# Kernel tuning notes

Hardware: AMD Instinct MI355X
Metric: run time of the kernel (lower is better)

Reference implementation:

```python
import jax, jax.numpy as jnp
import numpy as np

N_NODES = 50000
N_EDGES = 800000
DIM = 128
N_LAYERS = 4
EPS = 1e-5  # BatchNorm1d default eps


def setup_inputs() -> dict:
    key = jax.random.key(0)
    k_x, k_e, k_w = jax.random.split(key, 3)
    x = jax.random.normal(k_x, (N_NODES, DIM), dtype=jnp.float32)
    edge_index = jax.random.randint(k_e, (2, N_EDGES), 0, N_NODES, dtype=jnp.int32)
    # stacked per-layer params (input_dim == hidden_dim == DIM)
    Ws = jax.random.normal(k_w, (N_LAYERS, DIM, DIM), dtype=jnp.float32) * (1.0 / np.sqrt(DIM))
    bs = jnp.zeros((N_LAYERS, DIM), jnp.float32)
    gammas = jnp.ones((N_LAYERS, DIM), jnp.float32)
    betas = jnp.zeros((N_LAYERS, DIM), jnp.float32)
    return {"x": x, "edge_index": edge_index, "Ws": Ws, "bs": bs,
            "gammas": gammas, "betas": betas}


def gcn_conv(x, W, b, src, dst, n):
    # PyG GCNConv: h = X W; out = D^{-1/2}(A+I)D^{-1/2} h + b
    h = x @ W                                       # [N, D]
    deg = jnp.zeros((n,), h.dtype).at[dst].add(1.0) + 1.0  # +1 self-loop
    dis = jax.lax.rsqrt(deg)                        # deg > 0 due to self-loops
    msg = h[src] * (dis[src] * dis[dst])[:, None]   # [E, D] gather + scale
    out = jnp.zeros_like(h).at[dst].add(msg)        # scatter-add aggregate
    out = out + h * (dis * dis)[:, None]            # self-loop term, norm = 1/deg
    return out + b


def batchnorm(z, gamma, beta):
    # BatchNorm1d training-mode math: batch mean, biased variance
    mu = z.mean(axis=0)
    var = z.var(axis=0)
    return (z - mu) * jax.lax.rsqrt(var + EPS) * gamma + beta


def reference(x, edge_index, Ws, bs, gammas, betas):
    src, dst = edge_index[0], edge_index[1]
    z = x
    for i in range(N_LAYERS):
        z = gcn_conv(z, Ws[i], bs[i], src, dst, z.shape[0])
        z = jax.nn.relu(z)
        z = batchnorm(z, gammas[i], betas[i])
        # Dropout: identity (eval mode / deterministic reference)
    return z
```

## Files before the change

kernel.cpp:

```cpp
#include <hip/hip_runtime.h>

#define N_NODES 50000
#define N_EDGES 800000
#define DIM 128
#define NLAYERS 4
#define BN_EPS 1e-5f
#define SCAN_BLOCKS 196
#define WS2 72

typedef __attribute__((ext_vector_type(8))) short short8;
typedef __attribute__((ext_vector_type(4))) float f32x4;

__device__ __forceinline__ float bf2f(unsigned short u){
    union { unsigned int i; float f; } x; x.i = ((unsigned int)u) << 16; return x.f;
}
__device__ __forceinline__ unsigned short f2bf(float f){
    union { float f; unsigned int i; } x; x.f = f;
    unsigned int lsb = (x.i >> 16) & 1u;
    unsigned int r = x.i + 0x7fffu + lsb;
    return (unsigned short)(r >> 16);
}

struct P4 { int2 a, b, c, d; };

__device__ __forceinline__ P4 loadP_mask(const int2* __restrict__ ep, int base,
                                         int sub, int lim){
    P4 p;
    int i0 = base + sub, i1 = base + 4 + sub, i2 = base + 8 + sub, i3 = base + 12 + sub;
    p.a = (i0 < lim) ? ep[i0] : make_int2(0, 0);
    p.b = (i1 < lim) ? ep[i1] : make_int2(0, 0);
    p.c = (i2 < lim) ? ep[i2] : make_int2(0, 0);
    p.d = (i3 < lim) ? ep[i3] : make_int2(0, 0);
    return p;
}
__device__ __forceinline__ P4 loadP_full(const int2* __restrict__ ep, int base,
                                         int sub){
    P4 p;
    p.a = ep[base + sub];
    p.b = ep[base + 4 + sub];
    p.c = ep[base + 8 + sub];
    p.d = ep[base + 12 + sub];
    return p;
}
__device__ __forceinline__ P4 loadP(const int2* __restrict__ ep, int base,
                                    int sub, int lim){
    if (lim - base >= 16) return loadP_full(ep, base, sub);
    return loadP_mask(ep, base, sub, lim);
}


__global__ __launch_bounds__(256) void k_zero(int* __restrict__ p, int n){
    int i = blockIdx.x * 256 + threadIdx.x;
    if (i < n) p[i] = 0;
}

__global__ __launch_bounds__(256) void k_count(const int* __restrict__ dst,
                                               int* __restrict__ degcnt){
    int e = blockIdx.x * 256 + threadIdx.x;
    if (e < N_EDGES) atomicAdd(&degcnt[dst[e]], 1);
}

__global__ __launch_bounds__(256) void k_scan1(const int* __restrict__ degcnt,
                                               int* __restrict__ rowptr,
                                               int* __restrict__ bsum,
                                               float* __restrict__ dis){
    __shared__ int tmp[256];
    int t = threadIdx.x;
    int i = blockIdx.x * 256 + t;
    int v = (i < N_NODES) ? degcnt[i] : 0;
    if (i < N_NODES) dis[i] = rsqrtf((float)v + 1.0f);
    tmp[t] = v;
    __syncthreads();
    #pragma unroll
    for (int off = 1; off < 256; off <<= 1){
        int u = (t >= off) ? tmp[t - off] : 0;
        __syncthreads();
        tmp[t] += u;
        __syncthreads();
    }
    if (i < N_NODES) rowptr[i] = tmp[t] - v;
    if (t == 255) bsum[blockIdx.x] = tmp[255];
}

__global__ __launch_bounds__(256) void k_scan3(const int* __restrict__ bsum,
                                               int* __restrict__ rowptr,
                                               int* __restrict__ wptr){
    __shared__ int tmp[256];
    int t = threadIdx.x;
    int v = (t < SCAN_BLOCKS) ? bsum[t] : 0;
    tmp[t] = v;
    __syncthreads();
    #pragma unroll
    for (int off = 1; off < 256; off <<= 1){
        int u = (t >= off) ? tmp[t - off] : 0;
        __syncthreads();
        tmp[t] += u;
        __syncthreads();
    }
    int boff = (blockIdx.x == 0) ? 0 : tmp[blockIdx.x - 1];
    int i = blockIdx.x * 256 + t;
    if (i < N_NODES){
        int r = rowptr[i] + boff;
        rowptr[i] = r; wptr[i] = r;
    }
    if (i == 0) rowptr[N_NODES] = N_EDGES;
}

__global__ __launch_bounds__(256) void k_fill(const int* __restrict__ src,
                                              const int* __restrict__ dst,
                                              const float* __restrict__ dis,
                                              int* __restrict__ wptr,
                                              int2* __restrict__ epair){
    int e = blockIdx.x * 256 + threadIdx.x;
    if (e < N_EDGES){
        int s = src[e], d = dst[e];
        float w = dis[s] * dis[d];
        int p = atomicAdd(&wptr[d], 1);
        int2 pr; pr.x = s; pr.y = __float_as_int(w);
        epair[p] = pr;
    }
}


template<int MODE>
__global__ __launch_bounds__(256) void k_wprep(const float* __restrict__ W,
                                               const float* __restrict__ stats,
                                               const float* __restrict__ gamma,
                                               const float* __restrict__ beta,
                                               short* __restrict__ whip,
                                               short* __restrict__ wlop,
                                               float* __restrict__ b2g){
    __shared__ float scs[DIM], shs[DIM];
    __shared__ float part[256];
    int tid = threadIdx.x;
    if (MODE == 1){
        if (tid < DIM){
            float mu  = stats[tid] * (1.0f / N_NODES);
            float var = stats[DIM + tid] * (1.0f / N_NODES) - mu * mu;
            float sc  = rsqrtf(var + BN_EPS) * gamma[tid];
            scs[tid] = sc;
            shs[tid] = beta[tid] - mu * sc;
        }
        __syncthreads();
    }
    if (blockIdx.x < 16){
        int j = blockIdx.x * 1024 + tid * 4;
        int k = j >> 7;
        int c0 = j & 127;
        float4 wv = *(const float4*)(W + k*DIM + c0);
        float sc = (MODE == 1) ? scs[k] : 1.0f;
        float v[4] = {wv.x*sc, wv.y*sc, wv.z*sc, wv.w*sc};
        int h = k >> 6, kk = k & 63;
        #pragma unroll
        for (int i = 0; i < 4; i++){
            unsigned short hi = f2bf(v[i]);
            float lo = v[i] - bf2f(hi);
            int d = h*8192 + (c0 + i)*64 + kk;
            whip[d] = (short)hi;
            wlop[d] = (short)f2bf(lo);
        }
    } else {
        if (MODE == 0){
            if (tid < DIM) b2g[tid] = 0.f;
        } else {
            int c = tid >> 1, hf = tid & 1;
            float acc = 0.f;
            int k0 = hf * 64;
            #pragma unroll 4
            for (int k = k0; k < k0 + 64; k++)
                acc = fmaf(shs[k], W[k*DIM + c], acc);
            part[tid] = acc;
            __syncthreads();
            if (tid < DIM) b2g[tid] = part[2*tid] + part[2*tid + 1];
        }
    }
}

template<int MODE>
__global__ __launch_bounds__(256) void k_gemm(const void* __restrict__ zraw,
                                              const short* __restrict__ whip,
                                              const short* __restrict__ wlop,
                                              const float* __restrict__ b2g,
                                              unsigned short* __restrict__ hb){
    __shared__ short whi[DIM * WS2];
    __shared__ short wlo[DIM * WS2];
    __shared__ float b2s[DIM];
    int tid = threadIdx.x;

    int lane = tid & 63;
    int wv   = tid >> 6;
    int m = lane & 15;
    int q = lane >> 4;
    int row0 = blockIdx.x * 64 + wv * 16;
    int arow = row0 + m;
    bool avalid = arow < N_NODES;

    f32x4 acc[8];
    #pragma unroll
    for (int t = 0; t < 8; t++) acc[t] = (f32x4){0.f, 0.f, 0.f, 0.f};

    int cs = tid >> 1, pp = tid & 1;

    #pragma unroll
    for (int half = 0; half < 2; half++){
        {
            const short8* sh_ = (const short8*)(whip + half*8192 + cs*64 + pp*32);
            const short8* sl_ = (const short8*)(wlop + half*8192 + cs*64 + pp*32);
            short8* dh = (short8*)&whi[cs*WS2 + pp*32];
            short8* dl = (short8*)&wlo[cs*WS2 + pp*32];
            dh[0] = sh_[0]; dh[1] = sh_[1]; dh[2] = sh_[2]; dh[3] = sh_[3];
            dl[0] = sl_[0]; dl[1] = sl_[1]; dl[2] = sl_[2]; dl[3] = sl_[3];
            if (half == 0 && tid < DIM) b2s[tid] = b2g[tid];
        }
        __syncthreads();

        #pragma unroll
        for (int gl2 = 0; gl2 < 2; gl2++){
            int gg = half*2 + gl2;
            short8 a = {0,0,0,0,0,0,0,0};
            if (avalid){
                if (MODE == 0){
                    const float* xp = (const float*)zraw + (size_t)arow*DIM + gg*32 + q*8;
                    float4 v0 = *(const float4*)xp;
                    float4 v1 = *(const float4*)(xp + 4);
                    a[0] = (short)f2bf(v0.x); a[1] = (short)f2bf(v0.y);
                    a[2] = (short)f2bf(v0.z); a[3] = (short)f2bf(v0.w);
                    a[4] = (short)f2bf(v1.x); a[5] = (short)f2bf(v1.y);
                    a[6] = (short)f2bf(v1.z); a[7] = (short)f2bf(v1.w);
                } else {
                    a = *(const short8*)((const unsigned short*)zraw
                          + (size_t)gg*N_NODES*32 + (size_t)arow*32 + q*8);
                }
            }
            #pragma unroll
            for (int t = 0; t < 8; t++){
                int col = t*16 + m;
                int off = col*WS2 + gl2*32 + q*8;
                short8 bh = *(const short8*)&whi[off];
                short8 bl = *(const short8*)&wlo[off];
                acc[t] = __builtin_amdgcn_mfma_f32_16x16x32_bf16(a, bh, acc[t], 0, 0, 0);
                acc[t] = __builtin_amdgcn_mfma_f32_16x16x32_bf16(a, bl, acc[t], 0, 0, 0);
            }
        }
        if (half == 0) __syncthreads();
    }

    #pragma unroll
    for (int t = 0; t < 8; t++){
        int colg = t*16 + m;
        float bz = b2s[colg];
        size_t base = (size_t)(t >> 1)*N_NODES*32 + (t & 1)*16 + m;
        #pragma unroll
        for (int r = 0; r < 4; r++){
            int row = row0 + q*4 + r;
            if (row < N_NODES)
                hb[base + (size_t)row*32] = f2bf(acc[t][r] + bz);
        }
    }
}

__global__ __launch_bounds__(256) void k_agg(const unsigned short* __restrict__ h,
                                             const int* __restrict__ rowptr,
                                             const int2* __restrict__ epair,
                                             const float* __restrict__ dis,
                                             const float* __restrict__ bias,
                                             unsigned short* __restrict__ out,
                                             float* __restrict__ stats){
    int lane = threadIdx.x & 63;
    int w    = threadIdx.x >> 6;
    int g    = blockIdx.x & 3;
    int sub  = lane >> 4;
    int cp   = lane & 15;
    const ushort2* hg = (const ushort2*)(h + (size_t)g * N_NODES * 32);
    ushort2* og = (ushort2*)(out + (size_t)g * N_NODES * 32);
    float b0 = bias[g*32 + 2*cp], b1 = bias[g*32 + 2*cp + 1];
    float s0 = 0.f, s1 = 0.f, q0 = 0.f, q1 = 0.f;
    int bg = blockIdx.x >> 2;
    int nstride = (gridDim.x >> 2) * 4;

    int node = bg*4 + w;
    int ne0 = 0, ne1 = 0;
    ushort2 nhv; nhv.x = 0; nhv.y = 0;
    float ndi = 0.f;
    P4 nP = {{0,0},{0,0},{0,0},{0,0}};
    if (node < N_NODES){
        ne0 = rowptr[node];
        ne1 = rowptr[node + 1];
        nhv = hg[node*16 + cp];
        ndi = dis[node];
        nP  = loadP(epair, ne0, sub, ne1);
    }

    while (node < N_NODES){
        int e0 = ne0, e1 = ne1;
        ushort2 hv = nhv;
        float di = ndi;
        P4 P = nP;

        int nnext = node + nstride;
        if (nnext < N_NODES){
            ne0 = rowptr[nnext];
            ne1 = rowptr[nnext + 1];
            nhv = hg[nnext*16 + cp];
            ndi = dis[nnext];
        } else { ne0 = 0; ne1 = 0; }

        float pa0 = 0.f, pa1 = 0.f, pb0 = 0.f, pb1 = 0.f;
        float pc0 = 0.f, pc1 = 0.f, pd0 = 0.f, pd1 = 0.f;
        if (sub == 0){
            float dii = di * di;
            pa0 = bf2f(hv.x) * dii; pa1 = bf2f(hv.y) * dii;
        }

        int e = e0;
        while (e < e1){
            int en = e + 16;
            P4 Pn = {{0,0},{0,0},{0,0},{0,0}};
            if (en < e1) Pn = loadP(epair, en, sub, e1);
            ushort2 X0 = hg[P.a.x*16 + cp];
            ushort2 X1 = hg[P.b.x*16 + cp];
            ushort2 X2 = hg[P.c.x*16 + cp];
            ushort2 X3 = hg[P.d.x*16 + cp];
            float w0 = __int_as_float(P.a.y), w1 = __int_as_float(P.b.y);
            float w2 = __int_as_float(P.c.y), w3 = __int_as_float(P.d.y);
            pa0 = fmaf(bf2f(X0.x), w0, pa0); pa1 = fmaf(bf2f(X0.y), w0, pa1);
            pb0 = fmaf(bf2f(X1.x), w1, pb0); pb1 = fmaf(bf2f(X1.y), w1, pb1);
            pc0 = fmaf(bf2f(X2.x), w2, pc0); pc1 = fmaf(bf2f(X2.y), w2, pc1);
            pd0 = fmaf(bf2f(X3.x), w3, pd0); pd1 = fmaf(bf2f(X3.y), w3, pd1);
            P = Pn;
            e = en;
        }

        float r0 = (pa0 + pb0) + (pc0 + pd0);
        float r1 = (pa1 + pb1) + (pc1 + pd1);
        r0 += __shfl_xor(r0, 16); r1 += __shfl_xor(r1, 16);
        r0 += __shfl_xor(r0, 32); r1 += __shfl_xor(r1, 32);
        if (sub == 0){
            float a0 = fmaxf(r0 + b0, 0.f);
            float a1 = fmaxf(r1 + b1, 0.f);
            ushort2 ov; ov.x = f2bf(a0); ov.y = f2bf(a1);
            og[node*16 + cp] = ov;
            s0 += a0; s1 += a1; q0 += a0*a0; q1 += a1*a1;
        }

        if (nnext < N_NODES)
            nP = loadP(epair, ne0, sub, ne1);
        node = nnext;
    }

    __shared__ float red[4][16][4];
    if (sub == 0){
        red[w][cp][0] = s0; red[w][cp][1] = s1;
        red[w][cp][2] = q0; red[w][cp][3] = q1;
    }
    __syncthreads();
    if (w == 0 && sub == 0){
        #pragma unroll
        for (int ww = 1; ww < 4; ww++){
            s0 += red[ww][cp][0]; s1 += red[ww][cp][1];
            q0 += red[ww][cp][2]; q1 += red[ww][cp][3];
        }
        int c = g*32 + 2*cp;
        atomicAdd(&stats[c],         s0);
        atomicAdd(&stats[c + 1],     s1);
        atomicAdd(&stats[DIM + c],     q0);
        atomicAdd(&stats[DIM + c + 1], q1);
    }
}

__global__ __launch_bounds__(256) void k_bn(const uint4* __restrict__ in,
                                            const float* __restrict__ stats,
                                            const float* __restrict__ gamma,
                                            const float* __restrict__ beta,
                                            float4* __restrict__ outf){
    __shared__ float scs[DIM], shs[DIM];
    int tid = threadIdx.x;
    if (tid < DIM){
        float mu  = stats[tid] * (1.0f / N_NODES);
        float var = stats[DIM + tid] * (1.0f / N_NODES) - mu * mu;
        float sc  = rsqrtf(var + BN_EPS) * gamma[tid];
        scs[tid] = sc;
        shs[tid] = beta[tid] - mu * sc;
    }
    __syncthreads();

    int i = blockIdx.x * 256 + tid;
    if (i >= N_NODES * DIM / 8) return;
    int row = i >> 4;
    int c = (i * 8) & (DIM - 1);
    int gg = c >> 5, wi = c & 31;
    uint4 raw = in[gg*(N_NODES*4) + row*4 + (wi >> 3)];
    unsigned int u[4] = {raw.x, raw.y, raw.z, raw.w};
    float v[8];
    #pragma unroll
    for (int j = 0; j < 4; j++){
        v[2*j]   = bf2f((unsigned short)(u[j] & 0xffff));
        v[2*j+1] = bf2f((unsigned short)(u[j] >> 16));
    }
    float4 r0, r1;
    r0.x = fmaf(v[0], scs[c+0], shs[c+0]);
    r0.y = fmaf(v[1], scs[c+1], shs[c+1]);
    r0.z = fmaf(v[2], scs[c+2], shs[c+2]);
    r0.w = fmaf(v[3], scs[c+3], shs[c+3]);
    r1.x = fmaf(v[4], scs[c+4], shs[c+4]);
    r1.y = fmaf(v[5], scs[c+5], shs[c+5]);
    r1.z = fmaf(v[6], scs[c+6], shs[c+6]);
    r1.w = fmaf(v[7], scs[c+7], shs[c+7]);
    outf[2*i]   = r0;
    outf[2*i+1] = r1;
}


extern "C" void kernel_launch(void* const* d_in, const int* in_sizes, int n_in,
                              void* d_out, int out_size, void* d_ws, size_t ws_size,
                              hipStream_t stream){
    const float* x   = (const float*)d_in[0];
    const int*   src = (const int*)d_in[1];
    const int*   dst = src + N_EDGES;
    const float* Ws  = (const float*)d_in[2];
    const float* bs  = (const float*)d_in[3];
    const float* gs  = (const float*)d_in[4];
    const float* be  = (const float*)d_in[5];

    char* w = (char*)d_ws;
    int*   degcnt = (int*)(w);
    short* whip   = (short*)(w);
    short* wlop   = (short*)(w + 32768);
    float* b2g    = (float*)(w + 65536);
    float* stats  = (float*)(w + 200000);
    float* dis    = (float*)(w + 208192);
    int*   rowptr = (int*)(w + 408192);
    int*   wptr   = (int*)(w + 608208);
    int*   bsum   = (int*)(w + 808208);
    int2*  epair  = (int2*)(w + 875280);
    unsigned short* bufA = (unsigned short*)(w + 7275280);
    unsigned short* hb   = (unsigned short*)(w + 20075280);

    k_zero<<<(51024 + 255)/256, 256, 0, stream>>>(degcnt, 51024);
    k_count<<<3125, 256, 0, stream>>>(dst, degcnt);
    k_scan1<<<SCAN_BLOCKS, 256, 0, stream>>>(degcnt, rowptr, bsum, dis);
    k_scan3<<<SCAN_BLOCKS, 256, 0, stream>>>(bsum, rowptr, wptr);
    k_fill<<<3125, 256, 0, stream>>>(src, dst, dis, wptr, epair);

    for (int L = 0; L < NLAYERS; L++){
        const float* Wl = Ws + L*DIM*DIM;
        if (L == 0){
            k_wprep<0><<<17, 256, 0, stream>>>(Wl, nullptr, nullptr, nullptr,
                                               whip, wlop, b2g);
            k_gemm<0><<<(N_NODES + 63)/64, 256, 0, stream>>>(x, whip, wlop,
                                               b2g, hb);
        } else {
            k_wprep<1><<<17, 256, 0, stream>>>(Wl, stats + (L-1)*256,
                                               gs + (L-1)*DIM, be + (L-1)*DIM,
                                               whip, wlop, b2g);
            k_gemm<1><<<(N_NODES + 63)/64, 256, 0, stream>>>(bufA, whip, wlop,
                                               b2g, hb);
        }
        k_agg<<<2048, 256, 0, stream>>>(hb, rowptr, epair, dis, bs + L*DIM,
                                        bufA, stats + L*256);
    }
    k_bn<<<3125, 256, 0, stream>>>((const uint4*)bufA, stats + 3*256,
                                   gs + 3*DIM, be + 3*DIM, (float4*)d_out);
}
```

Before: 552.7 us.

## Prefetch next node's first neighbor feature gathers and pre-scale source indices

The aggregation kernel now prefetches both the edge pairs and the gathered neighbor feature values of the next node's first 16-edge chunk, overlapping those dependent loads with the current node's reduction and store. Edges beyond the first chunk are processed without the previous one-ahead epair prefetch. Source indices are stored pre-multiplied by the 64-byte row stride, so gathers use byte offsets and skip an index multiply. This trades more live registers, and possibly lower occupancy, for shorter dependent-load latency chains on typical low-degree nodes.

```diff
diff --git a/kernel.cpp b/kernel.cpp
--- a/kernel.cpp
+++ b/kernel.cpp
@@ -116,7 +116,7 @@
         int s = src[e], d = dst[e];
         float w = dis[s] * dis[d];
         int p = atomicAdd(&wptr[d], 1);
-        int2 pr; pr.x = s; pr.y = __float_as_int(w);
+        int2 pr; pr.x = s << 6; pr.y = __float_as_int(w);
         epair[p] = pr;
     }
 }
@@ -271,7 +271,8 @@
     int g    = blockIdx.x & 3;
     int sub  = lane >> 4;
     int cp   = lane & 15;
-    const ushort2* hg = (const ushort2*)(h + (size_t)g * N_NODES * 32);
+    int cp4  = cp * 4;
+    const char* hgb = (const char*)(h + (size_t)g * N_NODES * 32);
     ushort2* og = (ushort2*)(out + (size_t)g * N_NODES * 32);
     float b0 = bias[g*32 + 2*cp], b1 = bias[g*32 + 2*cp + 1];
     float s0 = 0.f, s1 = 0.f, q0 = 0.f, q1 = 0.f;
@@ -279,31 +280,34 @@
     int nstride = (gridDim.x >> 2) * 4;
 
     int node = bg*4 + w;
-    int ne0 = 0, ne1 = 0;
-    ushort2 nhv; nhv.x = 0; nhv.y = 0;
-    float ndi = 0.f;
-    P4 nP = {{0,0},{0,0},{0,0},{0,0}};
+    int e0 = 0, e1 = 0;
+    ushort2 hv; hv.x = 0; hv.y = 0;
+    float di = 0.f;
+    P4 P = {{0,0},{0,0},{0,0},{0,0}};
+    ushort2 X0 = {0,0}, X1 = {0,0}, X2 = {0,0}, X3 = {0,0};
     if (node < N_NODES){
-        ne0 = rowptr[node];
-        ne1 = rowptr[node + 1];
-        nhv = hg[node*16 + cp];
-        ndi = dis[node];
-        nP  = loadP(epair, ne0, sub, ne1);
+        e0 = rowptr[node];
+        e1 = rowptr[node + 1];
+        hv = *(const ushort2*)(hgb + (size_t)node*64 + cp4);
+        di = dis[node];
+        P  = loadP(epair, e0, sub, e1);
+        X0 = *(const ushort2*)(hgb + P.a.x + cp4);
+        X1 = *(const ushort2*)(hgb + P.b.x + cp4);
+        X2 = *(const ushort2*)(hgb + P.c.x + cp4);
+        X3 = *(const ushort2*)(hgb + P.d.x + cp4);
     }
 
     while (node < N_NODES){
-        int e0 = ne0, e1 = ne1;
-        ushort2 hv = nhv;
-        float di = ndi;
-        P4 P = nP;
-
         int nnext = node + nstride;
+        int ne0 = 0, ne1 = 0;
+        ushort2 nhv; nhv.x = 0; nhv.y = 0;
+        float ndi = 0.f;
         if (nnext < N_NODES){
             ne0 = rowptr[nnext];
             ne1 = rowptr[nnext + 1];
-            nhv = hg[nnext*16 + cp];
+            nhv = *(const ushort2*)(hgb + (size_t)nnext*64 + cp4);
             ndi = dis[nnext];
-        } else { ne0 = 0; ne1 = 0; }
+        }
 
         float pa0 = 0.f, pa1 = 0.f, pb0 = 0.f, pb1 = 0.f;
         float pc0 = 0.f, pc1 = 0.f, pd0 = 0.f, pd1 = 0.f;
@@ -311,30 +315,45 @@
             float dii = di * di;
             pa0 = bf2f(hv.x) * dii; pa1 = bf2f(hv.y) * dii;
         }
-
-        int e = e0;
-        while (e < e1){
-            int en = e + 16;
-            P4 Pn = {{0,0},{0,0},{0,0},{0,0}};
-            if (en < e1) Pn = loadP(epair, en, sub, e1);
-            ushort2 X0 = hg[P.a.x*16 + cp];
-            ushort2 X1 = hg[P.b.x*16 + cp];
-            ushort2 X2 = hg[P.c.x*16 + cp];
-            ushort2 X3 = hg[P.d.x*16 + cp];
+        {
             float w0 = __int_as_float(P.a.y), w1 = __int_as_float(P.b.y);
             float w2 = __int_as_float(P.c.y), w3 = __int_as_float(P.d.y);
             pa0 = fmaf(bf2f(X0.x), w0, pa0); pa1 = fmaf(bf2f(X0.y), w0, pa1);
             pb0 = fmaf(bf2f(X1.x), w1, pb0); pb1 = fmaf(bf2f(X1.y), w1, pb1);
             pc0 = fmaf(bf2f(X2.x), w2, pc0); pc1 = fmaf(bf2f(X2.y), w2, pc1);
             pd0 = fmaf(bf2f(X3.x), w3, pd0); pd1 = fmaf(bf2f(X3.y), w3, pd1);
-            P = Pn;
-            e = en;
+        }
+
+        P4 nP = {{0,0},{0,0},{0,0},{0,0}};
+        if (nnext < N_NODES) nP = loadP(epair, ne0, sub, ne1);
+
+        for (int e = e0 + 16; e < e1; e += 16){
+            P4 Q = loadP(epair, e, sub, e1);
+            ushort2 Y0 = *(const ushort2*)(hgb + Q.a.x + cp4);
+            ushort2 Y1 = *(const ushort2*)(hgb + Q.b.x + cp4);
+            ushort2 Y2 = *(const ushort2*)(hgb + Q.c.x + cp4);
+            ushort2 Y3 = *(const ushort2*)(hgb + Q.d.x + cp4);
+            float w0 = __int_as_float(Q.a.y), w1 = __int_as_float(Q.b.y);
+            float w2 = __int_as_float(Q.c.y), w3 = __int_as_float(Q.d.y);
+            pa0 = fmaf(bf2f(Y0.x), w0, pa0); pa1 = fmaf(bf2f(Y0.y), w0, pa1);
+            pb0 = fmaf(bf2f(Y1.x), w1, pb0); pb1 = fmaf(bf2f(Y1.y), w1, pb1);
+            pc0 = fmaf(bf2f(Y2.x), w2, pc0); pc1 = fmaf(bf2f(Y2.y), w2, pc1);
+            pd0 = fmaf(bf2f(Y3.x), w3, pd0); pd1 = fmaf(bf2f(Y3.y), w3, pd1);
         }
 
         float r0 = (pa0 + pb0) + (pc0 + pd0);
         float r1 = (pa1 + pb1) + (pc1 + pd1);
         r0 += __shfl_xor(r0, 16); r1 += __shfl_xor(r1, 16);
         r0 += __shfl_xor(r0, 32); r1 += __shfl_xor(r1, 32);
+
+        ushort2 nX0 = {0,0}, nX1 = {0,0}, nX2 = {0,0}, nX3 = {0,0};
+        if (nnext < N_NODES){
+            nX0 = *(const ushort2*)(hgb + nP.a.x + cp4);
+            nX1 = *(const ushort2*)(hgb + nP.b.x + cp4);
+            nX2 = *(const ushort2*)(hgb + nP.c.x + cp4);
+            nX3 = *(const ushort2*)(hgb + nP.d.x + cp4);
+        }
+
         if (sub == 0){
             float a0 = fmaxf(r0 + b0, 0.f);
             float a1 = fmaxf(r1 + b1, 0.f);
@@ -343,8 +362,9 @@
             s0 += a0; s1 += a1; q0 += a0*a0; q1 += a1*a1;
         }
 
-        if (nnext < N_NODES)
-            nP = loadP(epair, ne0, sub, ne1);
+        e0 = ne0; e1 = ne1; hv = nhv; di = ndi;
+        P = nP;
+        X0 = nX0; X1 = nX1; X2 = nX2; X3 = nX3;
         node = nnext;
     }
 
```

Result: no change. 549.4 us (-0.6%).

## Deepen software pipeline in aggregation kernel across three nodes

Applied to the files above, without the earlier changes.

The aggregation loop now prefetches row pointers three nodes ahead, edge pairs two nodes ahead, and the first chunk of gathered neighbor features one node ahead, rotating registers each iteration. This hides gather latency for the common case where a node has at most 16 edges. Source indices are stored pre-shifted by 6 as byte offsets, so address calculation skips a multiply. The cost is higher register pressure, and the tail chunks of high-degree nodes are no longer prefetched.

```diff
diff --git a/kernel.cpp b/kernel.cpp
--- a/kernel.cpp
+++ b/kernel.cpp
@@ -116,7 +116,7 @@
         int s = src[e], d = dst[e];
         float w = dis[s] * dis[d];
         int p = atomicAdd(&wptr[d], 1);
-        int2 pr; pr.x = s; pr.y = __float_as_int(w);
+        int2 pr; pr.x = s << 6; pr.y = __float_as_int(w);
         epair[p] = pr;
     }
 }
@@ -271,81 +271,95 @@
     int g    = blockIdx.x & 3;
     int sub  = lane >> 4;
     int cp   = lane & 15;
-    const ushort2* hg = (const ushort2*)(h + (size_t)g * N_NODES * 32);
+    int cp4  = cp * 4;
+    const char* hgb = (const char*)(h + (size_t)g * N_NODES * 32);
     ushort2* og = (ushort2*)(out + (size_t)g * N_NODES * 32);
     float b0 = bias[g*32 + 2*cp], b1 = bias[g*32 + 2*cp + 1];
     float s0 = 0.f, s1 = 0.f, q0 = 0.f, q1 = 0.f;
     int bg = blockIdx.x >> 2;
-    int nstride = (gridDim.x >> 2) * 4;
-
-    int node = bg*4 + w;
-    int ne0 = 0, ne1 = 0;
-    ushort2 nhv; nhv.x = 0; nhv.y = 0;
-    float ndi = 0.f;
-    P4 nP = {{0,0},{0,0},{0,0},{0,0}};
-    if (node < N_NODES){
-        ne0 = rowptr[node];
-        ne1 = rowptr[node + 1];
-        nhv = hg[node*16 + cp];
-        ndi = dis[node];
-        nP  = loadP(epair, ne0, sub, ne1);
-    }
-
-    while (node < N_NODES){
-        int e0 = ne0, e1 = ne1;
-        ushort2 hv = nhv;
-        float di = ndi;
-        P4 P = nP;
-
-        int nnext = node + nstride;
-        if (nnext < N_NODES){
-            ne0 = rowptr[nnext];
-            ne1 = rowptr[nnext + 1];
-            nhv = hg[nnext*16 + cp];
-            ndi = dis[nnext];
-        } else { ne0 = 0; ne1 = 0; }
-
-        float pa0 = 0.f, pa1 = 0.f, pb0 = 0.f, pb1 = 0.f;
-        float pc0 = 0.f, pc1 = 0.f, pd0 = 0.f, pd1 = 0.f;
+    int S = (gridDim.x >> 2) * 4;
+
+    int n0 = bg*4 + w;
+    int n1 = n0 + S, n2 = n1 + S;
+
+    int e00=0,e01=0; ushort2 hv0={0,0}; float di0=0.f;
+    if (n0 < N_NODES){ e00=rowptr[n0]; e01=rowptr[n0+1];
+        hv0=*(const ushort2*)(hgb+(size_t)n0*64+cp4); di0=dis[n0]; }
+    int e10=0,e11=0; ushort2 hv1={0,0}; float di1=0.f;
+    if (n1 < N_NODES){ e10=rowptr[n1]; e11=rowptr[n1+1];
+        hv1=*(const ushort2*)(hgb+(size_t)n1*64+cp4); di1=dis[n1]; }
+    int e20=0,e21=0; ushort2 hv2={0,0}; float di2=0.f;
+    if (n2 < N_NODES){ e20=rowptr[n2]; e21=rowptr[n2+1];
+        hv2=*(const ushort2*)(hgb+(size_t)n2*64+cp4); di2=dis[n2]; }
+    P4 P0={{0,0},{0,0},{0,0},{0,0}}, P1=P0;
+    if (n0 < N_NODES) P0 = loadP(epair, e00, sub, e01);
+    if (n1 < N_NODES) P1 = loadP(epair, e10, sub, e11);
+    ushort2 X0={0,0},X1={0,0},X2={0,0},X3={0,0};
+    if (n0 < N_NODES){
+        X0=*(const ushort2*)(hgb+P0.a.x+cp4);
+        X1=*(const ushort2*)(hgb+P0.b.x+cp4);
+        X2=*(const ushort2*)(hgb+P0.c.x+cp4);
+        X3=*(const ushort2*)(hgb+P0.d.x+cp4);
+    }
+
+    while (n0 < N_NODES){
+        int n3 = n2 + S;
+        int e30=0,e31=0; ushort2 hv3={0,0}; float di3=0.f;
+        if (n3 < N_NODES){ e30=rowptr[n3]; e31=rowptr[n3+1];
+            hv3=*(const ushort2*)(hgb+(size_t)n3*64+cp4); di3=dis[n3]; }
+        P4 P2={{0,0},{0,0},{0,0},{0,0}};
+        if (n2 < N_NODES) P2 = loadP(epair, e20, sub, e21);
+        ushort2 Y0={0,0},Y1={0,0},Y2={0,0},Y3={0,0};
+        if (n1 < N_NODES){
+            Y0=*(const ushort2*)(hgb+P1.a.x+cp4);
+            Y1=*(const ushort2*)(hgb+P1.b.x+cp4);
+            Y2=*(const ushort2*)(hgb+P1.c.x+cp4);
+            Y3=*(const ushort2*)(hgb+P1.d.x+cp4);
+        }
+        float pa0=0.f,pa1=0.f,pb0=0.f,pb1=0.f;
+        float pc0=0.f,pc1=0.f,pd0=0.f,pd1=0.f;
         if (sub == 0){
-            float dii = di * di;
-            pa0 = bf2f(hv.x) * dii; pa1 = bf2f(hv.y) * dii;
-        }
-
-        int e = e0;
-        while (e < e1){
-            int en = e + 16;
-            P4 Pn = {{0,0},{0,0},{0,0},{0,0}};
-            if (en < e1) Pn = loadP(epair, en, sub, e1);
-            ushort2 X0 = hg[P.a.x*16 + cp];
-            ushort2 X1 = hg[P.b.x*16 + cp];
-            ushort2 X2 = hg[P.c.x*16 + cp];
-            ushort2 X3 = hg[P.d.x*16 + cp];
-            float w0 = __int_as_float(P.a.y), w1 = __int_as_float(P.b.y);
-            float w2 = __int_as_float(P.c.y), w3 = __int_as_float(P.d.y);
-            pa0 = fmaf(bf2f(X0.x), w0, pa0); pa1 = fmaf(bf2f(X0.y), w0, pa1);
-            pb0 = fmaf(bf2f(X1.x), w1, pb0); pb1 = fmaf(bf2f(X1.y), w1, pb1);
-            pc0 = fmaf(bf2f(X2.x), w2, pc0); pc1 = fmaf(bf2f(X2.y), w2, pc1);
-            pd0 = fmaf(bf2f(X3.x), w3, pd0); pd1 = fmaf(bf2f(X3.y), w3, pd1);
-            P = Pn;
-            e = en;
-        }
-
-        float r0 = (pa0 + pb0) + (pc0 + pd0);
-        float r1 = (pa1 + pb1) + (pc1 + pd1);
-        r0 += __shfl_xor(r0, 16); r1 += __shfl_xor(r1, 16);
-        r0 += __shfl_xor(r0, 32); r1 += __shfl_xor(r1, 32);
+            float dii = di0*di0;
+            pa0 = bf2f(hv0.x)*dii; pa1 = bf2f(hv0.y)*dii;
+        }
+        {
+            float w0=__int_as_float(P0.a.y), w1=__int_as_float(P0.b.y);
+            float w2=__int_as_float(P0.c.y), w3=__int_as_float(P0.d.y);
+            pa0=fmaf(bf2f(X0.x),w0,pa0); pa1=fmaf(bf2f(X0.y),w0,pa1);
+            pb0=fmaf(bf2f(X1.x),w1,pb0); pb1=fmaf(bf2f(X1.y),w1,pb1);
+            pc0=fmaf(bf2f(X2.x),w2,pc0); pc1=fmaf(bf2f(X2.y),w2,pc1);
+            pd0=fmaf(bf2f(X3.x),w3,pd0); pd1=fmaf(bf2f(X3.y),w3,pd1);
+        }
+        for (int e = e00 + 16; e < e01; e += 16){
+            P4 Q = loadP(epair, e, sub, e01);
+            ushort2 Z0=*(const ushort2*)(hgb+Q.a.x+cp4);
+            ushort2 Z1=*(const ushort2*)(hgb+Q.b.x+cp4);
+            ushort2 Z2=*(const ushort2*)(hgb+Q.c.x+cp4);
+            ushort2 Z3=*(const ushort2*)(hgb+Q.d.x+cp4);
+            float w0=__int_as_float(Q.a.y), w1=__int_as_float(Q.b.y);
+            float w2=__int_as_float(Q.c.y), w3=__int_as_float(Q.d.y);
+            pa0=fmaf(bf2f(Z0.x),w0,pa0); pa1=fmaf(bf2f(Z0.y),w0,pa1);
+            pb0=fmaf(bf2f(Z1.x),w1,pb0); pb1=fmaf(bf2f(Z1.y),w1,pb1);
+            pc0=fmaf(bf2f(Z2.x),w2,pc0); pc1=fmaf(bf2f(Z2.y),w2,pc1);
+            pd0=fmaf(bf2f(Z3.x),w3,pd0); pd1=fmaf(bf2f(Z3.y),w3,pd1);
+        }
+        float r0 = (pa0+pb0)+(pc0+pd0);
+        float r1 = (pa1+pb1)+(pc1+pd1);
+        r0 += __shfl_xor(r0,16); r1 += __shfl_xor(r1,16);
+        r0 += __shfl_xor(r0,32); r1 += __shfl_xor(r1,32);
         if (sub == 0){
-            float a0 = fmaxf(r0 + b0, 0.f);
-            float a1 = fmaxf(r1 + b1, 0.f);
-            ushort2 ov; ov.x = f2bf(a0); ov.y = f2bf(a1);
-            og[node*16 + cp] = ov;
-            s0 += a0; s1 += a1; q0 += a0*a0; q1 += a1*a1;
-        }
-
-        if (nnext < N_NODES)
-            nP = loadP(epair, ne0, sub, ne1);
-        node = nnext;
+            float a0 = fmaxf(r0+b0, 0.f);
+            float a1 = fmaxf(r1+b1, 0.f);
+            ushort2 ov; ov.x=f2bf(a0); ov.y=f2bf(a1);
+            og[n0*16+cp] = ov;
+            s0+=a0; s1+=a1; q0+=a0*a0; q1+=a1*a1;
+        }
+        e00=e10; e01=e11; hv0=hv1; di0=di1;
+        e10=e20; e11=e21; hv1=hv2; di1=di2;
+        e20=e30; e21=e31; hv2=hv3; di2=di3;
+        P0=P1; P1=P2;
+        X0=Y0; X1=Y1; X2=Y2; X3=Y3;
+        n0=n1; n1=n2; n2=n3;
     }
 
     __shared__ float red[4][16][4];
```

New measurement: 579.6 us. +4.9%, slower.

## Switch hidden features to row-major layout and wave-per-node aggregation with readlane broadcast

Applied to the files above, without the earlier changes.

Hidden activations change from a four-slab column-group layout to plain row-major bf16 rows in the GEMM, aggregation and BN kernels. Aggregation now has one wavefront per node covering all 128 columns: 16 edge pairs are loaded per lane group and broadcast with readlane, and each gather reads a full 256-byte row. Source indices are pre-shifted by 8 so they act as byte offsets. This removes the four-way column-group split (each edge list was read four times) and the cross-lane shuffle reduction, but drops the edge-list prefetch and the multiple independent accumulators, so there is less memory-level parallelism per wave.

```diff
diff --git a/kernel.cpp b/kernel.cpp
--- a/kernel.cpp
+++ b/kernel.cpp
@@ -19,33 +19,6 @@
     unsigned int lsb = (x.i >> 16) & 1u;
     unsigned int r = x.i + 0x7fffu + lsb;
     return (unsigned short)(r >> 16);
-}
-
-struct P4 { int2 a, b, c, d; };
-
-__device__ __forceinline__ P4 loadP_mask(const int2* __restrict__ ep, int base,
-                                         int sub, int lim){
-    P4 p;
-    int i0 = base + sub, i1 = base + 4 + sub, i2 = base + 8 + sub, i3 = base + 12 + sub;
-    p.a = (i0 < lim) ? ep[i0] : make_int2(0, 0);
-    p.b = (i1 < lim) ? ep[i1] : make_int2(0, 0);
-    p.c = (i2 < lim) ? ep[i2] : make_int2(0, 0);
-    p.d = (i3 < lim) ? ep[i3] : make_int2(0, 0);
-    return p;
-}
-__device__ __forceinline__ P4 loadP_full(const int2* __restrict__ ep, int base,
-                                         int sub){
-    P4 p;
-    p.a = ep[base + sub];
-    p.b = ep[base + 4 + sub];
-    p.c = ep[base + 8 + sub];
-    p.d = ep[base + 12 + sub];
-    return p;
-}
-__device__ __forceinline__ P4 loadP(const int2* __restrict__ ep, int base,
-                                    int sub, int lim){
-    if (lim - base >= 16) return loadP_full(ep, base, sub);
-    return loadP_mask(ep, base, sub, lim);
 }
 
 
@@ -116,7 +89,7 @@
         int s = src[e], d = dst[e];
         float w = dis[s] * dis[d];
         int p = atomicAdd(&wptr[d], 1);
-        int2 pr; pr.x = s; pr.y = __float_as_int(w);
+        int2 pr; pr.x = s << 8; pr.y = __float_as_int(w);
         epair[p] = pr;
     }
 }
@@ -229,7 +202,7 @@
                     a[6] = (short)f2bf(v1.z); a[7] = (short)f2bf(v1.w);
                 } else {
                     a = *(const short8*)((const unsigned short*)zraw
-                          + (size_t)gg*N_NODES*32 + (size_t)arow*32 + q*8);
+                          + (size_t)arow*DIM + gg*32 + q*8);
                 }
             }
             #pragma unroll
@@ -249,122 +222,92 @@
     for (int t = 0; t < 8; t++){
         int colg = t*16 + m;
         float bz = b2s[colg];
-        size_t base = (size_t)(t >> 1)*N_NODES*32 + (t & 1)*16 + m;
         #pragma unroll
         for (int r = 0; r < 4; r++){
             int row = row0 + q*4 + r;
             if (row < N_NODES)
-                hb[base + (size_t)row*32] = f2bf(acc[t][r] + bz);
-        }
-    }
-}
-
-__global__ __launch_bounds__(256) void k_agg(const unsigned short* __restrict__ h,
-                                             const int* __restrict__ rowptr,
-                                             const int2* __restrict__ epair,
-                                             const float* __restrict__ dis,
-                                             const float* __restrict__ bias,
-                                             unsigned short* __restrict__ out,
-                                             float* __restrict__ stats){
+                hb[(size_t)row*DIM + colg] = f2bf(acc[t][r] + bz);
+        }
+    }
+}
+
+__global__ __launch_bounds__(256) void k_aggr(const unsigned short* __restrict__ h,
+                                              const int* __restrict__ rowptr,
+                                              const int2* __restrict__ epair,
+                                              const float* __restrict__ dis,
+                                              const float* __restrict__ bias,
+                                              unsigned short* __restrict__ out,
+                                              float* __restrict__ stats){
     int lane = threadIdx.x & 63;
     int w    = threadIdx.x >> 6;
-    int g    = blockIdx.x & 3;
-    int sub  = lane >> 4;
-    int cp   = lane & 15;
-    const ushort2* hg = (const ushort2*)(h + (size_t)g * N_NODES * 32);
-    ushort2* og = (ushort2*)(out + (size_t)g * N_NODES * 32);
-    float b0 = bias[g*32 + 2*cp], b1 = bias[g*32 + 2*cp + 1];
-    float s0 = 0.f, s1 = 0.f, q0 = 0.f, q1 = 0.f;
-    int bg = blockIdx.x >> 2;
-    int nstride = (gridDim.x >> 2) * 4;
-
-    int node = bg*4 + w;
-    int ne0 = 0, ne1 = 0;
-    ushort2 nhv; nhv.x = 0; nhv.y = 0;
-    float ndi = 0.f;
-    P4 nP = {{0,0},{0,0},{0,0},{0,0}};
+    const char* hbb = (const char*)h;
+    char* ob = (char*)out;
+    float2 bl = *(const float2*)(bias + 2*lane);
+    float s0=0.f, s1=0.f, q0=0.f, q1=0.f;
+    int stride = (int)gridDim.x * 4;
+    int node = blockIdx.x * 4 + w;
+
+    int e0=0, e1=0; unsigned hv=0; float di=0.f;
     if (node < N_NODES){
-        ne0 = rowptr[node];
-        ne1 = rowptr[node + 1];
-        nhv = hg[node*16 + cp];
-        ndi = dis[node];
-        nP  = loadP(epair, ne0, sub, ne1);
+        e0 = rowptr[node]; e1 = rowptr[node+1];
+        hv = *(const unsigned*)(hbb + (size_t)node*256 + (lane<<2));
+        di = dis[node];
     }
 
     while (node < N_NODES){
-        int e0 = ne0, e1 = ne1;
-        ushort2 hv = nhv;
-        float di = ndi;
-        P4 P = nP;
-
-        int nnext = node + nstride;
-        if (nnext < N_NODES){
-            ne0 = rowptr[nnext];
-            ne1 = rowptr[nnext + 1];
-            nhv = hg[nnext*16 + cp];
-            ndi = dis[nnext];
-        } else { ne0 = 0; ne1 = 0; }
-
-        float pa0 = 0.f, pa1 = 0.f, pb0 = 0.f, pb1 = 0.f;
-        float pc0 = 0.f, pc1 = 0.f, pd0 = 0.f, pd1 = 0.f;
-        if (sub == 0){
-            float dii = di * di;
-            pa0 = bf2f(hv.x) * dii; pa1 = bf2f(hv.y) * dii;
-        }
-
-        int e = e0;
-        while (e < e1){
-            int en = e + 16;
-            P4 Pn = {{0,0},{0,0},{0,0},{0,0}};
-            if (en < e1) Pn = loadP(epair, en, sub, e1);
-            ushort2 X0 = hg[P.a.x*16 + cp];
-            ushort2 X1 = hg[P.b.x*16 + cp];
-            ushort2 X2 = hg[P.c.x*16 + cp];
-            ushort2 X3 = hg[P.d.x*16 + cp];
-            float w0 = __int_as_float(P.a.y), w1 = __int_as_float(P.b.y);
-            float w2 = __int_as_float(P.c.y), w3 = __int_as_float(P.d.y);
-            pa0 = fmaf(bf2f(X0.x), w0, pa0); pa1 = fmaf(bf2f(X0.y), w0, pa1);
-            pb0 = fmaf(bf2f(X1.x), w1, pb0); pb1 = fmaf(bf2f(X1.y), w1, pb1);
-            pc0 = fmaf(bf2f(X2.x), w2, pc0); pc1 = fmaf(bf2f(X2.y), w2, pc1);
-            pd0 = fmaf(bf2f(X3.x), w3, pd0); pd1 = fmaf(bf2f(X3.y), w3, pd1);
-            P = Pn;
-            e = en;
-        }
-
-        float r0 = (pa0 + pb0) + (pc0 + pd0);
-        float r1 = (pa1 + pb1) + (pc1 + pd1);
-        r0 += __shfl_xor(r0, 16); r1 += __shfl_xor(r1, 16);
-        r0 += __shfl_xor(r0, 32); r1 += __shfl_xor(r1, 32);
-        if (sub == 0){
-            float a0 = fmaxf(r0 + b0, 0.f);
-            float a1 = fmaxf(r1 + b1, 0.f);
-            ushort2 ov; ov.x = f2bf(a0); ov.y = f2bf(a1);
-            og[node*16 + cp] = ov;
-            s0 += a0; s1 += a1; q0 += a0*a0; q1 += a1*a1;
-        }
-
-        if (nnext < N_NODES)
-            nP = loadP(epair, ne0, sub, ne1);
-        node = nnext;
-    }
-
-    __shared__ float red[4][16][4];
-    if (sub == 0){
-        red[w][cp][0] = s0; red[w][cp][1] = s1;
-        red[w][cp][2] = q0; red[w][cp][3] = q1;
-    }
+        int nn = node + stride;
+        int ne0=0, ne1=0; unsigned nhv=0; float ndi=0.f;
+        if (nn < N_NODES){
+            ne0 = rowptr[nn]; ne1 = rowptr[nn+1];
+            nhv = *(const unsigned*)(hbb + (size_t)nn*256 + (lane<<2));
+            ndi = dis[nn];
+        }
+        float dii = di * di;
+        float a0 = __uint_as_float(hv << 16) * dii;
+        float a1 = __uint_as_float(hv & 0xffff0000u) * dii;
+
+        for (int e = e0; e < e1; e += 16){
+            int elane = e + (lane & 15);
+            int2 pe = (elane < e1) ? epair[elane] : make_int2(0, 0);
+            #pragma unroll
+            for (int jb = 0; jb < 4; jb++){
+                if (e + jb*4 < e1){
+                    #pragma unroll
+                    for (int j = jb*4; j < jb*4 + 4; j++){
+                        int sx = __builtin_amdgcn_readlane(pe.x, j);
+                        float wj = __int_as_float(
+                                     __builtin_amdgcn_readlane(pe.y, j));
+                        unsigned xv = *(const unsigned*)(hbb + sx + (lane<<2));
+                        a0 = fmaf(__uint_as_float(xv << 16),         wj, a0);
+                        a1 = fmaf(__uint_as_float(xv & 0xffff0000u), wj, a1);
+                    }
+                }
+            }
+        }
+
+        a0 = fmaxf(a0 + bl.x, 0.f);
+        a1 = fmaxf(a1 + bl.y, 0.f);
+        unsigned ov = ((unsigned)f2bf(a1) << 16) | (unsigned)f2bf(a0);
+        *(unsigned*)(ob + (size_t)node*256 + (lane<<2)) = ov;
+        s0 += a0; s1 += a1; q0 += a0*a0; q1 += a1*a1;
+
+        e0=ne0; e1=ne1; hv=nhv; di=ndi; node = nn;
+    }
+
+    __shared__ float red[4][64][4];
+    red[w][lane][0]=s0; red[w][lane][1]=s1;
+    red[w][lane][2]=q0; red[w][lane][3]=q1;
     __syncthreads();
-    if (w == 0 && sub == 0){
+    if (w == 0){
         #pragma unroll
         for (int ww = 1; ww < 4; ww++){
-            s0 += red[ww][cp][0]; s1 += red[ww][cp][1];
-            q0 += red[ww][cp][2]; q1 += red[ww][cp][3];
-        }
-        int c = g*32 + 2*cp;
-        atomicAdd(&stats[c],         s0);
-        atomicAdd(&stats[c + 1],     s1);
-        atomicAdd(&stats[DIM + c],     q0);
-        atomicAdd(&stats[DIM + c + 1], q1);
+            s0 += red[ww][lane][0]; s1 += red[ww][lane][1];
+            q0 += red[ww][lane][2]; q1 += red[ww][lane][3];
+        }
+        atomicAdd(&stats[2*lane],           s0);
+        atomicAdd(&stats[2*lane + 1],       s1);
+        atomicAdd(&stats[DIM + 2*lane],     q0);
+        atomicAdd(&stats[DIM + 2*lane + 1], q1);
     }
 }
 
@@ -386,10 +329,8 @@
 
     int i = blockIdx.x * 256 + tid;
     if (i >= N_NODES * DIM / 8) return;
-    int row = i >> 4;
     int c = (i * 8) & (DIM - 1);
-    int gg = c >> 5, wi = c & 31;
-    uint4 raw = in[gg*(N_NODES*4) + row*4 + (wi >> 3)];
+    uint4 raw = in[i];
     unsigned int u[4] = {raw.x, raw.y, raw.z, raw.w};
     float v[8];
     #pragma unroll
@@ -456,8 +397,8 @@
             k_gemm<1><<<(N_NODES + 63)/64, 256, 0, stream>>>(bufA, whip, wlop,
                                                b2g, hb);
         }
-        k_agg<<<2048, 256, 0, stream>>>(hb, rowptr, epair, dis, bs + L*DIM,
-                                        bufA, stats + L*256);
+        k_aggr<<<2048, 256, 0, stream>>>(hb, rowptr, epair, dis, bs + L*DIM,
+                                         bufA, stats + L*256);
     }
     k_bn<<<3125, 256, 0, stream>>>((const uint4*)bufA, stats + 3*256,
                                    gs + 3*DIM, be + 3*DIM, (float4*)d_out);
```

New measurement: 774.7 us. 40.2% more time.
